# Kernel optimization log

Measured on AMD Instinct MI355X. Metric: run time of the kernel, lower is better.

The kernel has to match this reference:

```python
import jax, jax.numpy as jnp
import numpy as np

N_EMBD = 1024
N_HEAD = 16
HEAD_DIM = N_EMBD // N_HEAD


def setup_inputs() -> dict:
    key = jax.random.key(0)
    kx, kq, kk, kv, ko = jax.random.split(key, 5)
    B, T = 4, 2048
    std = 1.0 / np.sqrt(N_EMBD)
    return {
        "x": jax.random.normal(kx, (B, T, N_EMBD), dtype=jnp.float32),
        "wq": jax.random.normal(kq, (N_EMBD, N_EMBD), dtype=jnp.float32) * std,
        "wk": jax.random.normal(kk, (N_EMBD, N_EMBD), dtype=jnp.float32) * std,
        "wv": jax.random.normal(kv, (N_EMBD, N_EMBD), dtype=jnp.float32) * std,
        "wo": jax.random.normal(ko, (N_EMBD, N_EMBD), dtype=jnp.float32) * std,
    }


def reference(x, wq, wk, wv, wo):
    B, T, C = x.shape
    # nn.Linear(x) = x @ W.T; weights stored as (out, in)
    def proj(w):
        return jnp.einsum('btc,dc->btd', x, w).reshape(B, T, N_HEAD, HEAD_DIM).transpose(0, 2, 1, 3)
    q, k, v = proj(wq), proj(wk), proj(wv)  # [B,H,T,Dh]
    scale = HEAD_DIM ** -0.5
    attn = jnp.einsum('bhtd,bhsd->bhts', q, k) * scale  # [B,H,T,T]
    causal = jnp.tril(jnp.ones((T, T), dtype=bool))
    attn = jnp.where(causal, attn, -jnp.inf)
    attn = jax.nn.softmax(attn, axis=-1)
    out = jnp.einsum('bhts,bhsd->bhtd', attn, v)  # [B,H,T,Dh]
    out = out.transpose(0, 2, 1, 3).reshape(B, T, C)
    return jnp.einsum('btc,dc->btd', out, wo)
```

## Files before the change

### kernel.cpp

```cpp
#include <hip/hip_runtime.h>
#include <hip/hip_bf16.h>
#include <stdint.h>

typedef __attribute__((ext_vector_type(8))) __bf16 bf16x8;
typedef __attribute__((ext_vector_type(4))) __bf16 bf16x4;
typedef __attribute__((ext_vector_type(4))) float  f32x4;

#define MFMA16(a, b, c) __builtin_amdgcn_mfma_f32_16x16x32_bf16((a), (b), (c), 0, 0, 0)

#define GLD16(gp, lp) __builtin_amdgcn_global_load_lds(                                   \
    (const __attribute__((address_space(1))) uint32_t*)(gp),                              \
    (__attribute__((address_space(3))) uint32_t*)(lp), 16, 0, 0)

#define BB 4
#define TT 2048
#define CC 1024
#define HH 16
#define DH 64
#define GM 8192
#define GN 1024
#define GK 1024

__global__ __launch_bounds__(256) void cvt_all_kernel(const float* __restrict__ x,
                                                      const float* __restrict__ w0,
                                                      const float* __restrict__ w1,
                                                      const float* __restrict__ w2,
                                                      const float* __restrict__ w3,
                                                      __bf16* __restrict__ xb,
                                                      __bf16* __restrict__ wb) {
    int gb = blockIdx.x;
    const float* src;
    __bf16* dst;
    int i;
    if (gb < 4096) {
        src = x; dst = xb;
        i = gb * 256 + threadIdx.x;
    } else {
        int g = gb - 4096;
        int wz = g >> 9, lb = g & 511;
        const float* srcs[4] = {w0, w1, w2, w3};
        src = srcs[wz]; dst = wb + (size_t)wz * CC * CC;
        i = lb * 256 + threadIdx.x;
    }
    const float4* s = (const float4*)src + (size_t)i * 2;
    float4 f0 = s[0], f1 = s[1];
    bf16x8 h;
    h[0] = (__bf16)f0.x; h[1] = (__bf16)f0.y; h[2] = (__bf16)f0.z; h[3] = (__bf16)f0.w;
    h[4] = (__bf16)f1.x; h[5] = (__bf16)f1.y; h[6] = (__bf16)f1.z; h[7] = (__bf16)f1.w;
    *(bf16x8*)(dst + (size_t)i * 8) = h;
}

__global__ __launch_bounds__(256) void transpose_kernel(const __bf16* __restrict__ V,
                                                        __bf16* __restrict__ VT) {
    __shared__ __bf16 Ts[64][72];
    int tid = threadIdx.x;
    int m0 = blockIdx.x * 64, c0 = blockIdx.y * 64;
#pragma unroll
    for (int r = 0; r < 2; r++) {
        int ch = r * 256 + tid;
        int mm = ch >> 3, c8 = (ch & 7) * 8;
        *(uint4*)&Ts[mm][c8] = *(const uint4*)(V + (size_t)(m0 + mm) * CC + c0 + c8);
    }
    __syncthreads();
#pragma unroll
    for (int r = 0; r < 2; r++) {
        int ch = r * 256 + tid;
        int cc = ch >> 3, m8 = (ch & 7) * 8;
        bf16x8 v;
#pragma unroll
        for (int e = 0; e < 8; e++) v[e] = Ts[m8 + e][cc];
        *(bf16x8*)(VT + (size_t)(c0 + cc) * GM + m0 + m8) = v;
    }
}

__global__ __launch_bounds__(256) void gemm_nt(const __bf16* __restrict__ A,
                                               const __bf16* __restrict__ Bmat,
                                               __bf16* __restrict__ Cbf,
                                               float* __restrict__ Cf,
                                               size_t b_zstride, size_t c_zstride) {
    int id = blockIdx.x;
    int xcd = id & 7;
    int slot = id >> 3;
    int z = slot >> 6;
    int rem = slot & 63;
    int mb = xcd * 8 + (rem >> 3);
    int nb = rem & 7;
    const __bf16* Bp = Bmat + (size_t)z * b_zstride;
    __shared__ __bf16 As[2 * 128 * 32];
    __shared__ __bf16 Bs[2 * 128 * 32];
    int tid  = threadIdx.x;
    int lane = tid & 63, w = tid >> 6;
    int wm = w >> 1, wn = w & 1;
    int l15 = lane & 15, q8 = lane >> 4;
    int m0 = mb * 128, n0 = nb * 128;

    f32x4 zero = {0.f, 0.f, 0.f, 0.f};
    f32x4 acc[4][4];
#pragma unroll
    for (int i = 0; i < 4; i++)
#pragma unroll
        for (int j = 0; j < 4; j++) acc[i][j] = zero;

    const __bf16* Ag[4];
    const __bf16* Bg[4];
#pragma unroll
    for (int t = 0; t < 4; t++) {
        int c = tid + 256 * t;
        int half = c >> 9, row = (c & 511) >> 2, kc = (c & 3) * 8;
        Ag[t] = A  + (size_t)(m0 + row) * GK + half * 32 + kc;
        Bg[t] = Bp + (size_t)(n0 + row) * GK + half * 32 + kc;
    }
    char* AsB = (char*)As; char* BsB = (char*)Bs;
    int wbase = (tid & ~63) * 16;

    for (int k0 = 0; k0 < GK; k0 += 64) {
        __syncthreads();
#pragma unroll
        for (int t = 0; t < 4; t++) {
            GLD16(Ag[t] + k0, AsB + t * 4096 + wbase);
            GLD16(Bg[t] + k0, BsB + t * 4096 + wbase);
        }
        __syncthreads();
#pragma unroll
        for (int kk = 0; kk < 2; kk++) {
            bf16x8 af[4], bf[4];
#pragma unroll
            for (int mt = 0; mt < 4; mt++)
                af[mt] = *(const bf16x8*)(As + kk * 4096 + (wm * 64 + mt * 16 + l15) * 32 + q8 * 8);
#pragma unroll
            for (int nt = 0; nt < 4; nt++)
                bf[nt] = *(const bf16x8*)(Bs + kk * 4096 + (wn * 64 + nt * 16 + l15) * 32 + q8 * 8);
#pragma unroll
            for (int mt = 0; mt < 4; mt++)
#pragma unroll
                for (int nt = 0; nt < 4; nt++)
                    acc[mt][nt] = MFMA16(af[mt], bf[nt], acc[mt][nt]);
        }
    }

#pragma unroll
    for (int mt = 0; mt < 4; mt++) {
        int mrow = m0 + wm * 64 + mt * 16 + q8 * 4;
#pragma unroll
        for (int nt = 0; nt < 4; nt++) {
            int ncol = n0 + wn * 64 + nt * 16 + l15;
            f32x4 v = acc[mt][nt];
            if (Cf) {
                float* p = Cf + (size_t)z * c_zstride + (size_t)mrow * GN + ncol;
                p[0] = v.x; p[GN] = v.y; p[2 * GN] = v.z; p[3 * GN] = v.w;
            } else {
                __bf16* p = Cbf + (size_t)z * c_zstride + (size_t)mrow * GN + ncol;
                p[0] = (__bf16)v.x; p[GN] = (__bf16)v.y;
                p[2 * GN] = (__bf16)v.z; p[3 * GN] = (__bf16)v.w;
            }
        }
    }
}

__global__ __launch_bounds__(256) void attn_kernel(const __bf16* __restrict__ Q,
                                                   const __bf16* __restrict__ K,
                                                   const __bf16* __restrict__ VT,
                                                   __bf16* __restrict__ Y) {
    __shared__ __bf16 Ks[2][64 * 64];
    __shared__ __bf16 Vs[2][64 * 64];
    __shared__ __bf16 Ps[4][16 * 64];

    int tid  = threadIdx.x;
    int lane = tid & 63, w = tid >> 6;
    int l15 = lane & 15, q8 = lane >> 4;
    int y  = blockIdx.y, y0 = y & 3, kk = y >> 2;
    int qt = (kk & 1) ? (2 * y0 + (kk >> 1)) : (15 - (kk >> 1) - 2 * y0);
    int bh = blockIdx.x, b = bh >> 4, h = bh & 15;
    size_t rowb = (size_t)b * TT;
    const float SC = 0.125f * 1.44269504f;
    const float M2 = 12.0f * 1.44269504f;
    int ql = w * 16 + l15;
    int x7 = l15 & 7;

    bf16x8 qfr[2][2];
#pragma unroll
    for (int qf = 0; qf < 2; qf++) {
        int q = qt * 128 + qf * 64 + w * 16 + l15;
        const __bf16* qp = Q + (rowb + q) * CC + h * DH + q8 * 8;
        bf16x8 r0 = *(const bf16x8*)qp;
        bf16x8 r1 = *(const bf16x8*)(qp + 32);
#pragma unroll
        for (int e = 0; e < 8; e++) {
            r0[e] = (__bf16)((float)r0[e] * SC);
            r1[e] = (__bf16)((float)r1[e] * SC);
        }
        qfr[qf][0] = r0; qfr[qf][1] = r1;
    }

    f32x4 zero = {0.f, 0.f, 0.f, 0.f};
    f32x4 acc[2][5];
#pragma unroll
    for (int qf = 0; qf < 2; qf++)
#pragma unroll
        for (int t5 = 0; t5 < 5; t5++) acc[qf][t5] = zero;

    bf16x8 ones;
#pragma unroll
    for (int e = 0; e < 8; e++) ones[e] = (l15 == 0) ? (__bf16)1.0f : (__bf16)0.0f;

    int c0 = tid, c1 = tid + 256;
    int s0 = c0 >> 3, d80 = ((c0 & 7) ^ (s0 & 7)) * 8;
    int s1 = c1 >> 3, d81 = ((c1 & 7) ^ (s1 & 7)) * 8;
    const __bf16* Kg0 = K + (rowb + s0) * CC + h * DH + d80;
    const __bf16* Kg1 = K + (rowb + s1) * CC + h * DH + d81;
    const __bf16* Vg0 = VT + (size_t)(h * DH + s0) * GM + rowb + d80;
    const __bf16* Vg1 = VT + (size_t)(h * DH + s1) * GM + rowb + d81;
    char* KsB = (char*)Ks; char* VsB = (char*)Vs;
    int wbase = (tid & ~63) * 16;

    GLD16(Kg0, KsB + wbase);
    GLD16(Kg1, KsB + 4096 + wbase);
    GLD16(Vg0, VsB + wbase);
    GLD16(Vg1, VsB + 4096 + wbase);

    int jmax = 2 * qt + 1;
    for (int j = 0; j <= jmax; j++) {
        __syncthreads();
        if (j < jmax) {
            int bo = ((j + 1) & 1) * 8192;
            GLD16(Kg0 + (size_t)(j + 1) * 64 * CC, KsB + bo + wbase);
            GLD16(Kg1 + (size_t)(j + 1) * 64 * CC, KsB + bo + 4096 + wbase);
            GLD16(Vg0 + (j + 1) * 64, VsB + bo + wbase);
            GLD16(Vg1 + (j + 1) * 64, VsB + bo + 4096 + wbase);
        }
        const __bf16* Kc = &Ks[j & 1][0];
        const __bf16* Vc = &Vs[j & 1][0];
        bool do0 = (j != jmax);

        f32x4 s2[2][4];
#pragma unroll
        for (int st = 0; st < 4; st++) {
            bf16x8 k0f = *(const bf16x8*)(Kc + (st * 16 + l15) * 64 + ((q8 ^ x7) * 8));
            bf16x8 k1f = *(const bf16x8*)(Kc + (st * 16 + l15) * 64 + (((q8 + 4) ^ x7) * 8));
            f32x4 t1 = zero;
            t1 = MFMA16(k0f, qfr[1][0], t1);
            t1 = MFMA16(k1f, qfr[1][1], t1);
            s2[1][st] = t1;
            if (do0) {
                f32x4 t0 = zero;
                t0 = MFMA16(k0f, qfr[0][0], t0);
                t0 = MFMA16(k1f, qfr[0][1], t0);
                s2[0][st] = t0;
            }
        }

#pragma unroll
        for (int qf = 0; qf < 2; qf++) {
            if (qf == 0 && !do0) continue;
            if (j == 2 * qt + qf) {
#pragma unroll
                for (int st = 0; st < 4; st++) {
                    f32x4 t = s2[qf][st];
                    int sb = st * 16 + q8 * 4;
                    t.x = (sb + 0 > ql) ? -1e30f : t.x;
                    t.y = (sb + 1 > ql) ? -1e30f : t.y;
                    t.z = (sb + 2 > ql) ? -1e30f : t.z;
                    t.w = (sb + 3 > ql) ? -1e30f : t.w;
                    s2[qf][st] = t;
                }
            }
        }

        bf16x8 bp[2][2];
#pragma unroll
        for (int qf = 0; qf < 2; qf++) {
            if (qf == 0 && !do0) continue;
#pragma unroll
            for (int st = 0; st < 4; st++) {
                bf16x4 pk;
                pk[0] = (__bf16)__builtin_amdgcn_exp2f(s2[qf][st].x - M2);
                pk[1] = (__bf16)__builtin_amdgcn_exp2f(s2[qf][st].y - M2);
                pk[2] = (__bf16)__builtin_amdgcn_exp2f(s2[qf][st].z - M2);
                pk[3] = (__bf16)__builtin_amdgcn_exp2f(s2[qf][st].w - M2);
                int swzc = (st * 2 + (q8 >> 1)) ^ x7;
                *(bf16x4*)(Ps[w] + l15 * 64 + swzc * 8 + (q8 & 1) * 4) = pk;
            }
            bp[qf][0] = *(const bf16x8*)(Ps[w] + l15 * 64 + ((q8 ^ x7) * 8));
            bp[qf][1] = *(const bf16x8*)(Ps[w] + l15 * 64 + (((q8 + 4) ^ x7) * 8));
        }

#pragma unroll
        for (int dt = 0; dt < 4; dt++) {
            bf16x8 v0 = *(const bf16x8*)(Vc + (dt * 16 + l15) * 64 + ((q8 ^ x7) * 8));
            bf16x8 v1 = *(const bf16x8*)(Vc + (dt * 16 + l15) * 64 + (((q8 + 4) ^ x7) * 8));
            acc[1][dt] = MFMA16(v0, bp[1][0], acc[1][dt]);
            acc[1][dt] = MFMA16(v1, bp[1][1], acc[1][dt]);
            if (do0) {
                acc[0][dt] = MFMA16(v0, bp[0][0], acc[0][dt]);
                acc[0][dt] = MFMA16(v1, bp[0][1], acc[0][dt]);
            }
        }
        acc[1][4] = MFMA16(ones, bp[1][0], acc[1][4]);
        acc[1][4] = MFMA16(ones, bp[1][1], acc[1][4]);
        if (do0) {
            acc[0][4] = MFMA16(ones, bp[0][0], acc[0][4]);
            acc[0][4] = MFMA16(ones, bp[0][1], acc[0][4]);
        }
    }

#pragma unroll
    for (int qf = 0; qf < 2; qf++) {
        float lsum = __shfl(acc[qf][4].x, l15);
        float ri = 1.0f / lsum;
        int q = qt * 128 + qf * 64 + w * 16 + l15;
        __bf16* yp = Y + (rowb + q) * CC + h * DH + q8 * 4;
#pragma unroll
        for (int dt = 0; dt < 4; dt++) {
            bf16x4 o;
            o[0] = (__bf16)(acc[qf][dt].x * ri);
            o[1] = (__bf16)(acc[qf][dt].y * ri);
            o[2] = (__bf16)(acc[qf][dt].z * ri);
            o[3] = (__bf16)(acc[qf][dt].w * ri);
            *(bf16x4*)(yp + dt * 16) = o;
        }
    }
}

extern "C" void kernel_launch(void* const* d_in, const int* in_sizes, int n_in,
                              void* d_out, int out_size, void* d_ws, size_t ws_size,
                              hipStream_t stream) {
    const float* x  = (const float*)d_in[0];
    const float* wq = (const float*)d_in[1];
    const float* wk = (const float*)d_in[2];
    const float* wv = (const float*)d_in[3];
    const float* wo = (const float*)d_in[4];
    float* out = (float*)d_out;

    char* ws = (char*)d_ws;
    __bf16* xb  = (__bf16*)ws;
    __bf16* wb  = (__bf16*)(ws + (size_t)16777216);
    __bf16* qkv = (__bf16*)(ws + (size_t)25165824);
    __bf16* yb  = (__bf16*)(ws + (size_t)75497472);

    cvt_all_kernel<<<dim3(4096 + 4 * 512), 256, 0, stream>>>(x, wq, wk, wv, wo, xb, wb);
    gemm_nt<<<dim3(1536), 256, 0, stream>>>(
        xb, wb, qkv, nullptr, (size_t)CC * CC, (size_t)GM * GN);
    transpose_kernel<<<dim3(GM / 64, GN / 64), 256, 0, stream>>>(
        qkv + (size_t)2 * GM * GN, xb);
    attn_kernel<<<dim3(BB * HH, 16), 256, 0, stream>>>(
        qkv, qkv + (size_t)GM * GN, xb, yb);
    gemm_nt<<<dim3(512), 256, 0, stream>>>(
        yb, wb + (size_t)3 * CC * CC, nullptr, out, 0, 0);
}
```

Baseline: 248.8 us.

## Replace QKV and output GEMM with 8-wave 256x128 software-pipelined kernel

Replaces the 128x128, 4-wave GEMM with a 512-thread kernel computing 256x128 tiles. Global-to-LDS loads are double buffered and interleaved with MFMA phases, using fine-grained barriers, s_setprio around MFMA bursts and vmcnt waits. The LDS layout is XOR-swizzled to avoid bank conflicts. The QKV projection now runs as one flat 8192x3072 problem instead of z-batched launches, and the XCD-aware block mapping is kept. The aim is to hide load latency and raise MFMA utilisation, at the cost of 96KB LDS per block, heavier register use and a more fragile hand-written schedule.

```diff
diff --git a/kernel.cpp b/kernel.cpp
--- a/kernel.cpp
+++ b/kernel.cpp
@@ -73,26 +73,38 @@
     }
 }
 
-__global__ __launch_bounds__(256) void gemm_nt(const __bf16* __restrict__ A,
-                                               const __bf16* __restrict__ Bmat,
-                                               __bf16* __restrict__ Cbf,
-                                               float* __restrict__ Cf,
-                                               size_t b_zstride, size_t c_zstride) {
+__global__ __launch_bounds__(512, 2) void gemm8(const __bf16* __restrict__ A,
+                                                const __bf16* __restrict__ Bmat,
+                                                __bf16* __restrict__ Cbf,
+                                                float* __restrict__ Cf) {
+    __shared__ __align__(16) char lds[98304];
+    char* ldsA = lds;
+    char* ldsB = lds + 65536;
+
     int id = blockIdx.x;
-    int xcd = id & 7;
-    int slot = id >> 3;
-    int z = slot >> 6;
-    int rem = slot & 63;
-    int mb = xcd * 8 + (rem >> 3);
-    int nb = rem & 7;
-    const __bf16* Bp = Bmat + (size_t)z * b_zstride;
-    __shared__ __bf16 As[2 * 128 * 32];
-    __shared__ __bf16 Bs[2 * 128 * 32];
+    int xcd = id & 7, slot = id >> 3;
+    int mb = xcd * 4 + (slot & 3);
+    int nb = slot >> 2;
+    int m0 = mb * 256, n0 = nb * 128;
+
     int tid  = threadIdx.x;
     int lane = tid & 63, w = tid >> 6;
     int wm = w >> 1, wn = w & 1;
     int l15 = lane & 15, q8 = lane >> 4;
-    int m0 = mb * 128, n0 = nb * 128;
+    int x7  = l15 & 7;
+
+    int arow = tid >> 3;
+    int lc   = (tid & 7) ^ (arow & 7);
+    const __bf16* Abase = A    + (size_t)(m0 + arow) * GK + lc * 8;
+    const __bf16* Bbase = Bmat + (size_t)(n0 + arow) * GK + lc * 8;
+    int wbase = (tid & ~63) * 16;
+
+    int cb0 = ((q8)     ^ x7) * 16;
+    int cb1 = ((q8 + 4) ^ x7) * 16;
+    int arb0 = (wm * 32 + l15) * 128;
+    int arb1 = (wm * 32 + 16 + l15) * 128;
+    int brb0 = (wn * 32 + l15) * 128;
+    int brb1 = (wn * 32 + 16 + l15) * 128;
 
     f32x4 zero = {0.f, 0.f, 0.f, 0.f};
     f32x4 acc[4][4];
@@ -101,60 +113,111 @@
 #pragma unroll
         for (int j = 0; j < 4; j++) acc[i][j] = zero;
 
-    const __bf16* Ag[4];
-    const __bf16* Bg[4];
-#pragma unroll
-    for (int t = 0; t < 4; t++) {
-        int c = tid + 256 * t;
-        int half = c >> 9, row = (c & 511) >> 2, kc = (c & 3) * 8;
-        Ag[t] = A  + (size_t)(m0 + row) * GK + half * 32 + kc;
-        Bg[t] = Bp + (size_t)(n0 + row) * GK + half * 32 + kc;
-    }
-    char* AsB = (char*)As; char* BsB = (char*)Bs;
-    int wbase = (tid & ~63) * 16;
-
-    for (int k0 = 0; k0 < GK; k0 += 64) {
-        __syncthreads();
-#pragma unroll
-        for (int t = 0; t < 4; t++) {
-            GLD16(Ag[t] + k0, AsB + t * 4096 + wbase);
-            GLD16(Bg[t] + k0, BsB + t * 4096 + wbase);
-        }
-        __syncthreads();
-#pragma unroll
-        for (int kk = 0; kk < 2; kk++) {
-            bf16x8 af[4], bf[4];
-#pragma unroll
-            for (int mt = 0; mt < 4; mt++)
-                af[mt] = *(const bf16x8*)(As + kk * 4096 + (wm * 64 + mt * 16 + l15) * 32 + q8 * 8);
-#pragma unroll
-            for (int nt = 0; nt < 4; nt++)
-                bf[nt] = *(const bf16x8*)(Bs + kk * 4096 + (wn * 64 + nt * 16 + l15) * 32 + q8 * 8);
-#pragma unroll
-            for (int mt = 0; mt < 4; mt++)
-#pragma unroll
-                for (int nt = 0; nt < 4; nt++)
-                    acc[mt][nt] = MFMA16(af[mt], bf[nt], acc[mt][nt]);
-        }
-    }
-
+    bf16x8 areg[2][2];
+    bf16x8 breg[4][2];
+
+#define STAGE_A(T_, H_) do {                                                              \
+        const __bf16* _g = Abase + (size_t)((H_) * 128) * GK + (((T_) & 15) * 64);        \
+        char* _d = ldsA + ((((T_) & 1) * 2 + (H_)) * 16384) + wbase;                      \
+        GLD16(_g, _d);                                                                    \
+        GLD16(_g + (size_t)64 * GK, _d + 8192);                                           \
+    } while (0)
+#define STAGE_B(T_, H_) do {                                                              \
+        const __bf16* _g = Bbase + (size_t)((H_) * 64) * GK + (((T_) & 15) * 64);         \
+        GLD16(_g, ldsB + ((((T_) & 1) * 2 + (H_)) * 8192) + wbase);                       \
+    } while (0)
+#define LD_A(BK_, H_) do {                                                                \
+        char* _p = ldsA + (((BK_) * 2 + (H_)) * 16384);                                   \
+        areg[0][0] = *(const bf16x8*)(_p + arb0 + cb0);                                   \
+        areg[0][1] = *(const bf16x8*)(_p + arb0 + cb1);                                   \
+        areg[1][0] = *(const bf16x8*)(_p + arb1 + cb0);                                   \
+        areg[1][1] = *(const bf16x8*)(_p + arb1 + cb1);                                   \
+    } while (0)
+#define LD_B(BK_, H_) do {                                                                \
+        char* _p = ldsB + (((BK_) * 2 + (H_)) * 8192);                                    \
+        breg[(H_) * 2 + 0][0] = *(const bf16x8*)(_p + brb0 + cb0);                        \
+        breg[(H_) * 2 + 0][1] = *(const bf16x8*)(_p + brb0 + cb1);                        \
+        breg[(H_) * 2 + 1][0] = *(const bf16x8*)(_p + brb1 + cb0);                        \
+        breg[(H_) * 2 + 1][1] = *(const bf16x8*)(_p + brb1 + cb1);                        \
+    } while (0)
+#define QMFMA(MH_, N0_, N1_) do {                                                         \
+        acc[(MH_)*2+0][N0_] = MFMA16(areg[0][0], breg[N0_][0], acc[(MH_)*2+0][N0_]);      \
+        acc[(MH_)*2+0][N1_] = MFMA16(areg[0][0], breg[N1_][0], acc[(MH_)*2+0][N1_]);      \
+        acc[(MH_)*2+1][N0_] = MFMA16(areg[1][0], breg[N0_][0], acc[(MH_)*2+1][N0_]);      \
+        acc[(MH_)*2+1][N1_] = MFMA16(areg[1][0], breg[N1_][0], acc[(MH_)*2+1][N1_]);      \
+        acc[(MH_)*2+0][N0_] = MFMA16(areg[0][1], breg[N0_][1], acc[(MH_)*2+0][N0_]);      \
+        acc[(MH_)*2+0][N1_] = MFMA16(areg[0][1], breg[N1_][1], acc[(MH_)*2+0][N1_]);      \
+        acc[(MH_)*2+1][N0_] = MFMA16(areg[1][1], breg[N0_][1], acc[(MH_)*2+1][N0_]);      \
+        acc[(MH_)*2+1][N1_] = MFMA16(areg[1][1], breg[N1_][1], acc[(MH_)*2+1][N1_]);      \
+    } while (0)
+#define BAR   __builtin_amdgcn_s_barrier()
+#define PRIO1 __builtin_amdgcn_s_setprio(1)
+#define PRIO0 __builtin_amdgcn_s_setprio(0)
+#define VM5   asm volatile("s_waitcnt vmcnt(5)" ::: "memory")
+
+    STAGE_A(0, 0); STAGE_A(0, 1); STAGE_B(0, 0); STAGE_B(0, 1);
+    STAGE_A(1, 0); STAGE_B(1, 1); STAGE_A(1, 1);
+    VM5;
+    BAR;
+
+    for (int i = 0; i < 8; i++) {
+        int t = 2 * i;
+        LD_A(0, 0); LD_B(0, 0);
+        STAGE_B(t + 1, 0);
+        BAR; PRIO1; QMFMA(0, 0, 1); PRIO0; BAR;
+        LD_B(0, 1);
+        STAGE_A(t + 2, 0);
+        BAR; PRIO1; QMFMA(0, 2, 3); PRIO0; BAR;
+        LD_A(0, 1);
+        STAGE_B(t + 2, 1);
+        BAR; PRIO1; QMFMA(1, 2, 3); PRIO0; BAR;
+        STAGE_A(t + 2, 1);
+        BAR; PRIO1; QMFMA(1, 0, 1); PRIO0;
+        VM5; BAR;
+        LD_A(1, 0); LD_B(1, 0);
+        STAGE_B(t + 2, 0);
+        BAR; PRIO1; QMFMA(0, 0, 1); PRIO0; BAR;
+        LD_B(1, 1);
+        STAGE_A(t + 3, 0);
+        BAR; PRIO1; QMFMA(0, 2, 3); PRIO0; BAR;
+        LD_A(1, 1);
+        STAGE_B(t + 3, 1);
+        BAR; PRIO1; QMFMA(1, 2, 3); PRIO0; BAR;
+        STAGE_A(t + 3, 1);
+        BAR; PRIO1; QMFMA(1, 0, 1); PRIO0;
+        VM5; BAR;
+    }
+
+    asm volatile("s_waitcnt vmcnt(0)" ::: "memory");
+
+    int zc  = n0 >> 10;
+    int ncb = n0 & 1023;
 #pragma unroll
     for (int mt = 0; mt < 4; mt++) {
-        int mrow = m0 + wm * 64 + mt * 16 + q8 * 4;
+        int mrow = m0 + (mt >> 1) * 128 + wm * 32 + (mt & 1) * 16 + q8 * 4;
 #pragma unroll
         for (int nt = 0; nt < 4; nt++) {
-            int ncol = n0 + wn * 64 + nt * 16 + l15;
+            int ncol = ncb + (nt >> 1) * 64 + wn * 32 + (nt & 1) * 16 + l15;
             f32x4 v = acc[mt][nt];
             if (Cf) {
-                float* p = Cf + (size_t)z * c_zstride + (size_t)mrow * GN + ncol;
+                float* p = Cf + (size_t)mrow * GN + ncol;
                 p[0] = v.x; p[GN] = v.y; p[2 * GN] = v.z; p[3 * GN] = v.w;
             } else {
-                __bf16* p = Cbf + (size_t)z * c_zstride + (size_t)mrow * GN + ncol;
+                __bf16* p = Cbf + (size_t)zc * ((size_t)GM * GN) + (size_t)mrow * GN + ncol;
                 p[0] = (__bf16)v.x; p[GN] = (__bf16)v.y;
                 p[2 * GN] = (__bf16)v.z; p[3 * GN] = (__bf16)v.w;
             }
         }
     }
+#undef STAGE_A
+#undef STAGE_B
+#undef LD_A
+#undef LD_B
+#undef QMFMA
+#undef BAR
+#undef PRIO1
+#undef PRIO0
+#undef VM5
 }
 
 __global__ __launch_bounds__(256) void attn_kernel(const __bf16* __restrict__ Q,
@@ -338,12 +401,10 @@
     __bf16* yb  = (__bf16*)(ws + (size_t)75497472);
 
     cvt_all_kernel<<<dim3(4096 + 4 * 512), 256, 0, stream>>>(x, wq, wk, wv, wo, xb, wb);
-    gemm_nt<<<dim3(1536), 256, 0, stream>>>(
-        xb, wb, qkv, nullptr, (size_t)CC * CC, (size_t)GM * GN);
+    gemm8<<<dim3(768), 512, 0, stream>>>(xb, wb, qkv, nullptr);
     transpose_kernel<<<dim3(GM / 64, GN / 64), 256, 0, stream>>>(
         qkv + (size_t)2 * GM * GN, xb);
     attn_kernel<<<dim3(BB * HH, 16), 256, 0, stream>>>(
         qkv, qkv + (size_t)GM * GN, xb, yb);
-    gemm_nt<<<dim3(512), 256, 0, stream>>>(
-        yb, wb + (size_t)3 * CC * CC, nullptr, out, 0, 0);
+    gemm8<<<dim3(256), 512, 0, stream>>>(yb, wb + (size_t)3 * CC * CC, nullptr, out);
 }
```

After: 245.6 us. No clear change (-1.3%).
